# Kernel optimization log

Measured on AMD Instinct MI355X. Metric: run time of the kernel, lower is better.

## Reference

```python
import jax, jax.numpy as jnp
import numpy as np

ALPHA = 0.2  # LeakyReLU negative slope (self.alpha)
NEG_INF = -1e9


def setup_inputs() -> dict:
    key = jax.random.key(0)
    k1, k2, k3, k4, k5 = jax.random.split(key, 5)
    N, Fin, Fout = 8192, 256, 128
    return {
        "input": jax.random.normal(k1, (N, Fin), dtype=jnp.float32),
        "W": jax.random.normal(k2, (Fin, Fout), dtype=jnp.float32) * 0.1,
        "c1": jax.random.normal(k3, (Fout, 1), dtype=jnp.float32) * 0.1,
        "c2": jax.random.normal(k4, (Fout, 1), dtype=jnp.float32) * 0.1,
        "adj": jax.random.randint(k5, (N, N), 0, 2, dtype=jnp.int32),
        "M": N,
    }


def reference(input, W, c1, c2, adj, M):
    # h: [N, Fout]
    h = input @ W
    # valid neighbor j for row x: adj[x, j] > 0 and h[j].sum() != 0
    valid = (adj[:M] > 0) & (jnp.sum(h, axis=1) != 0.0)[None, :]  # [M, N]
    # e[x, j] = leakyrelu(h[x] @ c1 + h[j] @ c2)
    s_dst = (h[:M] @ c1)            # [M, 1]
    s_src = (h @ c2).T              # [1, N]
    e = jax.nn.leaky_relu(s_dst + s_src, negative_slope=ALPHA)
    e = jnp.where(valid, e, NEG_INF)
    attn = jax.nn.softmax(e, axis=1)
    attn = jnp.where(valid, attn, 0.0)  # rows with no neighbors -> all-zero weights
    # dropout is identity at inference (training=False); pool=0 branch skipped
    h_prime = attn @ h              # [M, Fout]
    return jax.nn.elu(h_prime)
```

## Files before the change

### kernel.cpp

```cpp
#include <hip/hip_runtime.h>
#include <math.h>

typedef __attribute__((ext_vector_type(8))) short bf16x8;
typedef __attribute__((ext_vector_type(16))) float f32x16;

#define GAT_ALPHA 0.2f

static __device__ __forceinline__ unsigned short f2bf(float x) {
    unsigned u = __float_as_uint(x);
    u += 0x7fffu + ((u >> 16) & 1u);
    return (unsigned short)(u >> 16);
}
static __device__ __forceinline__ float bf2f(unsigned short b) {
    return __uint_as_float(((unsigned)b) << 16);
}

__global__ __launch_bounds__(512)
void k_prep(const float* __restrict__ input, const float* __restrict__ W,
            const float* __restrict__ c1, const float* __restrict__ c2,
            unsigned short* __restrict__ hb, float* __restrict__ ssx,
            float* __restrict__ sd, int N, int Fin, int Fout)
{
    __shared__ float in_lds[4][256];
    __shared__ float red[4][3];
    const int tid = threadIdx.x;
    const int r0 = blockIdx.x * 4;
    for (int idx = tid; idx < 4 * Fin; idx += 512) {
        int r = idx / Fin, c = idx - r * Fin;
        in_lds[r][c] = input[(size_t)(r0 + r) * Fin + c];
    }
    if (tid < 12) ((float*)red)[tid] = 0.f;
    __syncthreads();
    const int y = tid >> 7, f = tid & 127;
    float acc = 0.f;
    for (int k = 0; k < Fin; ++k)
        acc = fmaf(in_lds[y][k], W[(size_t)k * Fout + f], acc);
    const int row = r0 + y;
    hb[(size_t)row * Fout + f] = f2bf(acc);
    float rs = acc, sv = acc * c2[f], dv = acc * c1[f];
    for (int off = 32; off > 0; off >>= 1) {
        rs += __shfl_xor(rs, off);
        sv += __shfl_xor(sv, off);
        dv += __shfl_xor(dv, off);
    }
    if ((tid & 63) == 0) {
        atomicAdd(&red[y][0], rs);
        atomicAdd(&red[y][1], sv);
        atomicAdd(&red[y][2], dv);
    }
    __syncthreads();
    if (f == 0) {
        float rsum = red[y][0];
        ssx[row] = (rsum != 0.f) ? red[y][1] : -1e30f;
        sd[row]  = red[y][2];
    }
}

__global__ __launch_bounds__(1024)
void k_smax(const float* __restrict__ ssx, float* __restrict__ smax, int N)
{
    __shared__ float red[16];
    const int tid = threadIdx.x;
    float m = -3e38f;
    for (int i = tid; i < N; i += 1024) m = fmaxf(m, ssx[i]);
    for (int off = 32; off > 0; off >>= 1) m = fmaxf(m, __shfl_xor(m, off));
    if ((tid & 63) == 0) red[tid >> 6] = m;
    __syncthreads();
    if (tid == 0) {
        float mm = red[0];
        for (int i = 1; i < 16; ++i) mm = fmaxf(mm, red[i]);
        smax[0] = mm;
    }
}

__global__ __launch_bounds__(256)
void k_transpose(const unsigned short* __restrict__ hb, unsigned short* __restrict__ ht,
                 int N, int Fout)
{
    __shared__ unsigned short t[64][65];
    const int bx = blockIdx.x;
    const int by = blockIdx.y;
    const int tid = threadIdx.x;
    for (int i = 0; i < 16; ++i) {
        int idx = i * 256 + tid; int r = idx >> 6, c = idx & 63;
        t[r][c] = hb[(size_t)(bx * 64 + r) * Fout + by * 64 + c];
    }
    __syncthreads();
    for (int i = 0; i < 16; ++i) {
        int idx = i * 256 + tid; int r = idx >> 6, c = idx & 63;
        ht[(size_t)(by * 64 + r) * N + bx * 64 + c] = t[c][r];
    }
}

template<int JCH>
__global__ __launch_bounds__(256, 3)
void k_attn(const int* __restrict__ adj, const unsigned short* __restrict__ ht,
            const float* __restrict__ ssx, const float* __restrict__ sd,
            const float* __restrict__ smaxp, unsigned short* __restrict__ part,
            float* __restrict__ dpart, int N, int M)
{
    constexpr int WPR = JCH / 32;
    constexpr int NCH = JCH / 128;
    __shared__ unsigned bits[128 * WPR];
    __shared__ float sxl[JCH];
    __shared__ char btile[32768];

    const int tid = threadIdx.x;
    const int bi = blockIdx.x, bj = blockIdx.y;
    const int rb = bi * 128;
    const int j0 = bj * JCH;

    for (int i = tid * 4; i < JCH; i += 1024)
        *(float4*)&sxl[i] = *(const float4*)(ssx + j0 + i);

    {
        const int w4 = tid >> 6, lane = tid & 63;
        constexpr int IPASS = JCH / 512;
        unsigned char* bb8 = (unsigned char*)bits;
        for (int it = 0; it < 32; ++it) {
            const int r = it * 4 + w4;
            #pragma unroll
            for (int ps = 0; ps < IPASS; ++ps) {
                const int* __restrict__ ap =
                    adj + (size_t)(rb + r) * N + j0 + ps * 512 + lane * 8;
                int4 v0 = *(const int4*)ap;
                int4 v1 = *(const int4*)(ap + 4);
                unsigned b = (unsigned)(v0.x > 0)       | ((unsigned)(v0.y > 0) << 1)
                           | ((unsigned)(v0.z > 0) << 2) | ((unsigned)(v0.w > 0) << 3)
                           | ((unsigned)(v1.x > 0) << 4) | ((unsigned)(v1.y > 0) << 5)
                           | ((unsigned)(v1.z > 0) << 6) | ((unsigned)(v1.w > 0) << 7);
                const int wq = ps * 16 + (lane >> 2);
                bb8[r * (WPR * 4) + ((wq ^ (r & (WPR - 1))) << 2) + (lane & 3)] =
                    (unsigned char)b;
            }
        }
    }

    const int w = tid >> 6, l = tid & 63;
    const int col = l & 31, hi = l >> 5;
    const int rl = w * 32 + col;
    const int row = rb + rl;
    const float s0 = sd[row];
    const float vb = s0 + smaxp[0];
    const float m0 = fmaxf(vb, GAT_ALPHA * vb);

    const int fst = tid >> 1, hpart = tid & 1;
    const unsigned short* __restrict__ gst = ht + (size_t)fst * N + j0 + hpart * 64;
    char* const wbase = btile + fst * 256;
    const int fsw = fst & 7;

    const unsigned* __restrict__ brow = bits + rl * WPR;
    const int bswz = rl & (WPR - 1);
    const int soffbase = col & 7;

    f32x16 acc0 = {0,0,0,0,0,0,0,0,0,0,0,0,0,0,0,0};
    f32x16 acc1 = {0,0,0,0,0,0,0,0,0,0,0,0,0,0,0,0};
    f32x16 acc2 = {0,0,0,0,0,0,0,0,0,0,0,0,0,0,0,0};
    f32x16 acc3 = {0,0,0,0,0,0,0,0,0,0,0,0,0,0,0,0};
    float d0 = 0.f;

    __syncthreads();

    for (int ch = 0; ch < NCH; ++ch) {
        if (ch) __syncthreads();
        #pragma unroll
        for (int s = 0; s < 8; ++s) {
            bf16x8 v = *(const bf16x8*)(gst + ch * 128 + s * 8);
            *(bf16x8*)(wbase + (((hpart * 8 + s) ^ fsw) << 4)) = v;
        }
        __syncthreads();
        #pragma unroll
        for (int ks = 0; ks < 8; ++ks) {
            const unsigned bb = brow[(ch * 4 + (ks >> 1)) ^ bswz]
                                >> ((ks & 1) * 16 + hi * 8);
            const float* sx = &sxl[ch * 128 + ks * 16 + hi * 8];
            float4 x0 = *(const float4*)sx;
            float4 x1 = *(const float4*)(sx + 4);
            bf16x8 af;
            {
                unsigned short* pu = (unsigned short*)&af;
                const float* f0 = (const float*)&x0;
                const float* f1 = (const float*)&x1;
                float dd = 0.f;
                #pragma unroll
                for (int i = 0; i < 4; ++i) {
                    float v = s0 + f0[i];
                    float a = fmaxf(v, GAT_ALPHA * v);
                    float e = fminf(a - m0, 0.f);
                    float p = (bb & (1u << i)) ? __expf(e) : 0.f;
                    pu[i] = f2bf(p); dd += p;
                }
                #pragma unroll
                for (int i = 0; i < 4; ++i) {
                    float v = s0 + f1[i];
                    float a = fmaxf(v, GAT_ALPHA * v);
                    float e = fminf(a - m0, 0.f);
                    float p = (bb & (16u << i)) ? __expf(e) : 0.f;
                    pu[4 + i] = f2bf(p); dd += p;
                }
                d0 += dd;
            }
            const int soff = ((ks * 2 + hi) ^ soffbase) << 4;
            const char* bp = btile + col * 256 + soff;
            bf16x8 b0 = *(const bf16x8*)(bp);
            bf16x8 b1 = *(const bf16x8*)(bp + 8192);
            bf16x8 b2 = *(const bf16x8*)(bp + 16384);
            bf16x8 b3 = *(const bf16x8*)(bp + 24576);
            acc0 = __builtin_amdgcn_mfma_f32_32x32x16_bf16(af, b0, acc0, 0, 0, 0);
            acc1 = __builtin_amdgcn_mfma_f32_32x32x16_bf16(af, b1, acc1, 0, 0, 0);
            acc2 = __builtin_amdgcn_mfma_f32_32x32x16_bf16(af, b2, acc2, 0, 0, 0);
            acc3 = __builtin_amdgcn_mfma_f32_32x32x16_bf16(af, b3, acc3, 0, 0, 0);
        }
    }

    d0 += __shfl_xor(d0, 32);
    if (hi == 0) dpart[(size_t)bj * M + row] = d0;

    unsigned short* pb = part + (size_t)bj * M * 128
                       + (((size_t)(bi * 4 + w) * 256) + l) * 16;
    #define STORE_TILE(A, t) { \
        bf16x8 lo, hic; \
        unsigned short* q0 = (unsigned short*)&lo; \
        unsigned short* q1 = (unsigned short*)&hic; \
        q0[0]=f2bf(A[0]); q0[1]=f2bf(A[1]); q0[2]=f2bf(A[2]); q0[3]=f2bf(A[3]); \
        q0[4]=f2bf(A[4]); q0[5]=f2bf(A[5]); q0[6]=f2bf(A[6]); q0[7]=f2bf(A[7]); \
        q1[0]=f2bf(A[8]); q1[1]=f2bf(A[9]); q1[2]=f2bf(A[10]); q1[3]=f2bf(A[11]); \
        q1[4]=f2bf(A[12]); q1[5]=f2bf(A[13]); q1[6]=f2bf(A[14]); q1[7]=f2bf(A[15]); \
        *(bf16x8*)(pb + (size_t)(t) * 1024) = lo; \
        *(bf16x8*)(pb + (size_t)(t) * 1024 + 8) = hic; }
    STORE_TILE(acc0, 0)
    STORE_TILE(acc1, 1)
    STORE_TILE(acc2, 2)
    STORE_TILE(acc3, 3)
    #undef STORE_TILE
}

__global__ __launch_bounds__(256)
void k_dsum(const float* __restrict__ dpart, float* __restrict__ denom, int M, int nsp)
{
    const int r = blockIdx.x * 256 + threadIdx.x;
    if (r < M) {
        float d = 0.f;
        for (int s = 0; s < nsp; ++s) d += dpart[(size_t)s * M + r];
        denom[r] = d;
    }
}

__global__ __launch_bounds__(256)
void k_combine(const unsigned short* __restrict__ part, const float* __restrict__ denom,
               float* __restrict__ out, int M, int nsp)
{
    const int idx = blockIdx.x * 256 + threadIdx.x;
    const int s8 = idx & 1;
    const int l  = (idx >> 1) & 63;
    const int t  = (idx >> 7) & 3;
    const int w  = (idx >> 9) & 3;
    const int bi = idx >> 11;
    const int colg = t * 32 + (l & 31);
    const int hi = l >> 5;

    float sums[8] = {0.f, 0.f, 0.f, 0.f, 0.f, 0.f, 0.f, 0.f};
    const unsigned short* p = part + (size_t)idx * 8;
    for (int s = 0; s < nsp; ++s) {
        bf16x8 v = *(const bf16x8*)(p + (size_t)s * M * 128);
        const unsigned short* vp = (const unsigned short*)&v;
        #pragma unroll
        for (int i = 0; i < 8; ++i) sums[i] += bf2f(vp[i]);
    }
    const int rbase = bi * 128 + w * 32 + 4 * hi;
    #pragma unroll
    for (int i = 0; i < 8; ++i) {
        const int reg = s8 * 8 + i;
        const int row = rbase + (reg & 3) + 8 * (reg >> 2);
        const float dd = denom[row];
        const float inv = (dd > 0.f) ? 1.f / dd : 0.f;
        float x = sums[i] * inv;
        x = (x > 0.f) ? x : expm1f(x);
        out[(size_t)row * 128 + colg] = x;
    }
}

extern "C" void kernel_launch(void* const* d_in, const int* in_sizes, int n_in,
                              void* d_out, int out_size, void* d_ws, size_t ws_size,
                              hipStream_t stream)
{
    const float* input = (const float*)d_in[0];
    const float* W     = (const float*)d_in[1];
    const float* c1    = (const float*)d_in[2];
    const float* c2    = (const float*)d_in[3];
    const int*   adj   = (const int*)d_in[4];

    const int Fout = in_sizes[2];
    const int Fin  = in_sizes[1] / Fout;
    const int N    = in_sizes[0] / Fin;
    const int M    = out_size / Fout;
    float* out = (float*)d_out;

    char* ws = (char*)d_ws;
    const size_t o_hb   = 0;
    const size_t o_ht   = o_hb + (size_t)N * Fout * 2;
    const size_t o_ssx  = o_ht + (size_t)N * Fout * 2;
    const size_t o_sd   = o_ssx + (size_t)N * 4;
    const size_t o_smax = o_sd + (size_t)N * 4;
    const size_t o_den  = o_smax + 64;
    const size_t o_dpart = (o_den + (size_t)M * 4 + 63) & ~63ULL;

    int NS = 16;
    {
        size_t op16 = (o_dpart + (size_t)16 * M * 4 + 63) & ~63ULL;
        if (op16 + (size_t)16 * M * Fout * 2 > ws_size) NS = 8;
    }
    const size_t o_part = (o_dpart + (size_t)NS * M * 4 + 63) & ~63ULL;

    unsigned short* hb = (unsigned short*)(ws + o_hb);
    unsigned short* ht = (unsigned short*)(ws + o_ht);
    float* ssx   = (float*)(ws + o_ssx);
    float* sd    = (float*)(ws + o_sd);
    float* smax  = (float*)(ws + o_smax);
    float* denom = (float*)(ws + o_den);
    float* dpart = (float*)(ws + o_dpart);
    unsigned short* part = (unsigned short*)(ws + o_part);

    k_prep<<<N / 4, 512, 0, stream>>>(input, W, c1, c2, hb, ssx, sd, N, Fin, Fout);
    k_smax<<<1, 1024, 0, stream>>>(ssx, smax, N);
    k_transpose<<<dim3(N / 64, Fout / 64), 256, 0, stream>>>(hb, ht, N, Fout);

    if (NS == 16)
        k_attn<512><<<dim3(M / 128, 16), 256, 0, stream>>>(
            adj, ht, ssx, sd, smax, part, dpart, N, M);
    else
        k_attn<1024><<<dim3(M / 128, 8), 256, 0, stream>>>(
            adj, ht, ssx, sd, smax, part, dpart, N, M);

    k_dsum<<<(M + 255) / 256, 256, 0, stream>>>(dpart, denom, M, NS);
    k_combine<<<M * Fout / 8 / 256, 256, 0, stream>>>(part, denom, out, M, NS);
}
```

Baseline: 159.1 us.

## Double-buffer h tiles with register prefetch and stream adjacency directly per thread

Removes the upfront LDS bitmask build of the adjacency block and instead has each thread load its own adjacency row segments straight from global memory, prefetched two k-steps ahead in registers. The h^T tile staging is changed to 64-column chunks in a double-buffered LDS layout, with register prefetch two chunks ahead, and one barrier per chunk. The aim is to overlap global loads with MFMA work and drop the serial adjacency-packing phase. In exchange, per-thread adjacency loads are less coalesced (each lane reads its own row), register pressure rises, and the chunk count doubles.

```diff
diff --git a/kernel.cpp b/kernel.cpp
--- a/kernel.cpp
+++ b/kernel.cpp
@@ -99,11 +99,10 @@
             const float* __restrict__ smaxp, unsigned short* __restrict__ part,
             float* __restrict__ dpart, int N, int M)
 {
-    constexpr int WPR = JCH / 32;
-    constexpr int NCH = JCH / 128;
-    __shared__ unsigned bits[128 * WPR];
+    constexpr int NCH = JCH / 64;
+    constexpr int KSG = JCH / 16;
+    __shared__ char btile[2][16384];
     __shared__ float sxl[JCH];
-    __shared__ char btile[32768];
 
     const int tid = threadIdx.x;
     const int bi = blockIdx.x, bj = blockIdx.y;
@@ -113,45 +112,30 @@
     for (int i = tid * 4; i < JCH; i += 1024)
         *(float4*)&sxl[i] = *(const float4*)(ssx + j0 + i);
 
-    {
-        const int w4 = tid >> 6, lane = tid & 63;
-        constexpr int IPASS = JCH / 512;
-        unsigned char* bb8 = (unsigned char*)bits;
-        for (int it = 0; it < 32; ++it) {
-            const int r = it * 4 + w4;
-            #pragma unroll
-            for (int ps = 0; ps < IPASS; ++ps) {
-                const int* __restrict__ ap =
-                    adj + (size_t)(rb + r) * N + j0 + ps * 512 + lane * 8;
-                int4 v0 = *(const int4*)ap;
-                int4 v1 = *(const int4*)(ap + 4);
-                unsigned b = (unsigned)(v0.x > 0)       | ((unsigned)(v0.y > 0) << 1)
-                           | ((unsigned)(v0.z > 0) << 2) | ((unsigned)(v0.w > 0) << 3)
-                           | ((unsigned)(v1.x > 0) << 4) | ((unsigned)(v1.y > 0) << 5)
-                           | ((unsigned)(v1.z > 0) << 6) | ((unsigned)(v1.w > 0) << 7);
-                const int wq = ps * 16 + (lane >> 2);
-                bb8[r * (WPR * 4) + ((wq ^ (r & (WPR - 1))) << 2) + (lane & 3)] =
-                    (unsigned char)b;
-            }
-        }
-    }
-
     const int w = tid >> 6, l = tid & 63;
     const int col = l & 31, hi = l >> 5;
-    const int rl = w * 32 + col;
-    const int row = rb + rl;
+    const int row = rb + w * 32 + col;
     const float s0 = sd[row];
     const float vb = s0 + smaxp[0];
     const float m0 = fmaxf(vb, GAT_ALPHA * vb);
 
-    const int fst = tid >> 1, hpart = tid & 1;
-    const unsigned short* __restrict__ gst = ht + (size_t)fst * N + j0 + hpart * 64;
-    char* const wbase = btile + fst * 256;
-    const int fsw = fst & 7;
-
-    const unsigned* __restrict__ brow = bits + rl * WPR;
-    const int bswz = rl & (WPR - 1);
-    const int soffbase = col & 7;
+    const int L0 = 0 * 256 + tid, L1 = 1 * 256 + tid, L2 = 2 * 256 + tid, L3 = 3 * 256 + tid;
+    const unsigned short* sp0 = ht + (size_t)(L0 >> 3) * N + j0 + (((L0 & 7) ^ ((L0 >> 3) & 7)) << 3);
+    const unsigned short* sp1 = ht + (size_t)(L1 >> 3) * N + j0 + (((L1 & 7) ^ ((L1 >> 3) & 7)) << 3);
+    const unsigned short* sp2 = ht + (size_t)(L2 >> 3) * N + j0 + (((L2 & 7) ^ ((L2 >> 3) & 7)) << 3);
+    const unsigned short* sp3 = ht + (size_t)(L3 >> 3) * N + j0 + (((L3 & 7) ^ ((L3 >> 3) & 7)) << 3);
+
+    const int* __restrict__ abase = adj + (size_t)row * N + j0 + hi * 8;
+    int4 cA0 = *(const int4*)(abase);
+    int4 cA1 = *(const int4*)(abase + 4);
+    int4 cB0 = *(const int4*)(abase + 16);
+    int4 cB1 = *(const int4*)(abase + 20);
+
+    const int rswz = col & 7;
+    const char* const bb0 = (const char*)btile + (col + 0)  * 128;
+    const char* const bb1 = (const char*)btile + (col + 32) * 128;
+    const char* const bb2 = (const char*)btile + (col + 64) * 128;
+    const char* const bb3 = (const char*)btile + (col + 96) * 128;
 
     f32x16 acc0 = {0,0,0,0,0,0,0,0,0,0,0,0,0,0,0,0};
     f32x16 acc1 = {0,0,0,0,0,0,0,0,0,0,0,0,0,0,0,0};
@@ -159,26 +143,56 @@
     f32x16 acc3 = {0,0,0,0,0,0,0,0,0,0,0,0,0,0,0,0};
     float d0 = 0.f;
 
+    bf16x8 rr0 = *(const bf16x8*)(sp0);
+    bf16x8 rr1 = *(const bf16x8*)(sp1);
+    bf16x8 rr2 = *(const bf16x8*)(sp2);
+    bf16x8 rr3 = *(const bf16x8*)(sp3);
+    *(bf16x8*)(&btile[0][0] + L0 * 16) = rr0;
+    *(bf16x8*)(&btile[0][0] + L1 * 16) = rr1;
+    *(bf16x8*)(&btile[0][0] + L2 * 16) = rr2;
+    *(bf16x8*)(&btile[0][0] + L3 * 16) = rr3;
+    rr0 = *(const bf16x8*)(sp0 + 64);
+    rr1 = *(const bf16x8*)(sp1 + 64);
+    rr2 = *(const bf16x8*)(sp2 + 64);
+    rr3 = *(const bf16x8*)(sp3 + 64);
     __syncthreads();
 
     for (int ch = 0; ch < NCH; ++ch) {
-        if (ch) __syncthreads();
+        const int par = ch & 1;
+        if (ch + 1 < NCH) {
+            char* wb = &btile[par ^ 1][0];
+            *(bf16x8*)(wb + L0 * 16) = rr0;
+            *(bf16x8*)(wb + L1 * 16) = rr1;
+            *(bf16x8*)(wb + L2 * 16) = rr2;
+            *(bf16x8*)(wb + L3 * 16) = rr3;
+        }
+        if (ch + 2 < NCH) {
+            const int o = (ch + 2) * 64;
+            rr0 = *(const bf16x8*)(sp0 + o);
+            rr1 = *(const bf16x8*)(sp1 + o);
+            rr2 = *(const bf16x8*)(sp2 + o);
+            rr3 = *(const bf16x8*)(sp3 + o);
+        }
         #pragma unroll
-        for (int s = 0; s < 8; ++s) {
-            bf16x8 v = *(const bf16x8*)(gst + ch * 128 + s * 8);
-            *(bf16x8*)(wbase + (((hpart * 8 + s) ^ fsw) << 4)) = v;
-        }
-        __syncthreads();
-        #pragma unroll
-        for (int ks = 0; ks < 8; ++ks) {
-            const unsigned bb = brow[(ch * 4 + (ks >> 1)) ^ bswz]
-                                >> ((ks & 1) * 16 + hi * 8);
-            const float* sx = &sxl[ch * 128 + ks * 16 + hi * 8];
+        for (int ks = 0; ks < 4; ++ks) {
+            const int ksg = ch * 4 + ks;
+            int4 u0, u1;
+            if ((ks & 1) == 0) { u0 = cA0; u1 = cA1; }
+            else               { u0 = cB0; u1 = cB1; }
+            {
+                const int nk = (ksg + 2 < KSG) ? ksg + 2 : KSG - 1;
+                const int* np = abase + nk * 16;
+                if ((ks & 1) == 0) { cA0 = *(const int4*)np; cA1 = *(const int4*)(np + 4); }
+                else               { cB0 = *(const int4*)np; cB1 = *(const int4*)(np + 4); }
+            }
+            const float* sx = &sxl[ch * 64 + ks * 16 + hi * 8];
             float4 x0 = *(const float4*)sx;
             float4 x1 = *(const float4*)(sx + 4);
             bf16x8 af;
             {
                 unsigned short* pu = (unsigned short*)&af;
+                const int* ai0 = (const int*)&u0;
+                const int* ai1 = (const int*)&u1;
                 const float* f0 = (const float*)&x0;
                 const float* f1 = (const float*)&x1;
                 float dd = 0.f;
@@ -187,7 +201,7 @@
                     float v = s0 + f0[i];
                     float a = fmaxf(v, GAT_ALPHA * v);
                     float e = fminf(a - m0, 0.f);
-                    float p = (bb & (1u << i)) ? __expf(e) : 0.f;
+                    float p = (ai0[i] > 0) ? __expf(e) : 0.f;
                     pu[i] = f2bf(p); dd += p;
                 }
                 #pragma unroll
@@ -195,22 +209,22 @@
                     float v = s0 + f1[i];
                     float a = fmaxf(v, GAT_ALPHA * v);
                     float e = fminf(a - m0, 0.f);
-                    float p = (bb & (16u << i)) ? __expf(e) : 0.f;
+                    float p = (ai1[i] > 0) ? __expf(e) : 0.f;
                     pu[4 + i] = f2bf(p); dd += p;
                 }
                 d0 += dd;
             }
-            const int soff = ((ks * 2 + hi) ^ soffbase) << 4;
-            const char* bp = btile + col * 256 + soff;
-            bf16x8 b0 = *(const bf16x8*)(bp);
-            bf16x8 b1 = *(const bf16x8*)(bp + 8192);
-            bf16x8 b2 = *(const bf16x8*)(bp + 16384);
-            bf16x8 b3 = *(const bf16x8*)(bp + 24576);
+            const int soff = par * 16384 + (((ks * 2 + hi) ^ rswz) << 4);
+            bf16x8 b0 = *(const bf16x8*)(bb0 + soff);
+            bf16x8 b1 = *(const bf16x8*)(bb1 + soff);
+            bf16x8 b2 = *(const bf16x8*)(bb2 + soff);
+            bf16x8 b3 = *(const bf16x8*)(bb3 + soff);
             acc0 = __builtin_amdgcn_mfma_f32_32x32x16_bf16(af, b0, acc0, 0, 0, 0);
             acc1 = __builtin_amdgcn_mfma_f32_32x32x16_bf16(af, b1, acc1, 0, 0, 0);
             acc2 = __builtin_amdgcn_mfma_f32_32x32x16_bf16(af, b2, acc2, 0, 0, 0);
             acc3 = __builtin_amdgcn_mfma_f32_32x32x16_bf16(af, b3, acc3, 0, 0, 0);
         }
+        __syncthreads();
     }
 
     d0 += __shfl_xor(d0, 32);
```

New measurement: 139.4 us. -12.4%, faster.
